# Kernel optimization log

Measured on AMD Instinct MI355X. Metric: run time of the kernel, lower is better.

The kernel has to match this reference:

```python
import jax, jax.numpy as jnp
import numpy as np

GAMMA = 0.99
GAE_LAMBDA = 0.95
SEQ_LEN = 1024
BATCH = 32768


def setup_inputs() -> dict:
    key = jax.random.key(0)
    k1, k2 = jax.random.split(key)
    rewards = jax.random.normal(k1, (SEQ_LEN, BATCH), dtype=jnp.float32)
    values = jax.random.normal(k2, (SEQ_LEN, BATCH), dtype=jnp.float32)
    return {"rewards": rewards, "values": values}


def _compute_advantages(rewards, values, gamma, gae_lambda):
    # delta_t = r_t + gamma * V_{t+1} - V_t  for t = 0 .. T-2  -> [T-1, B]
    deltas = rewards[:-1] + gamma * values[1:] - values[:-1]
    gl = gamma * gae_lambda

    def step(carry, delta):
        adv = delta + gl * carry
        return adv, adv

    init = jnp.zeros_like(deltas[0])
    # reverse scan implements the backward-in-time GAE recurrence
    _, advantages = jax.lax.scan(step, init, deltas, reverse=True)
    return advantages  # [T-1, B], equals torch advantages[:-1]


def reference(rewards, values):
    return _compute_advantages(rewards, values, GAMMA, GAE_LAMBDA)
```

## Files before the change

### kernel.cpp

```cpp
#include <hip/hip_runtime.h>


#define GAE_T 1024
#define GAE_B 32768

__global__ __launch_bounds__(64) void gae_scan_kernel(
    const float* __restrict__ rewards,
    const float* __restrict__ values,
    float* __restrict__ out) {
    const int b = blockIdx.x * blockDim.x + threadIdx.x;

    const float gamma = 0.99f;
    const float gl = (float)(0.99 * 0.95);

    const float* rp = rewards + b;
    const float* vp = values + b;
    float* op = out + b;

    float v_next = vp[(GAE_T - 1) * GAE_B];
    float adv = 0.0f;

    int t = GAE_T - 2;

    for (int k = 0; k < 7; ++k, --t) {
        float v = vp[t * GAE_B];
        float r = rp[t * GAE_B];
        adv = r + gamma * v_next - v + gl * adv;
        op[t * GAE_B] = adv;
        v_next = v;
    }

    for (; t >= 7; t -= 8) {
        float r8[8], v8[8];
#pragma unroll
        for (int k = 0; k < 8; ++k) {
            v8[k] = vp[(t - k) * GAE_B];
            r8[k] = rp[(t - k) * GAE_B];
        }
#pragma unroll
        for (int k = 0; k < 8; ++k) {
            float v = v8[k];
            adv = r8[k] + gamma * v_next - v + gl * adv;
            op[(t - k) * GAE_B] = adv;
            v_next = v;
        }
    }
}

extern "C" void kernel_launch(void* const* d_in, const int* in_sizes, int n_in,
                              void* d_out, int out_size, void* d_ws, size_t ws_size,
                              hipStream_t stream) {
    const float* rewards = (const float*)d_in[0];
    const float* values = (const float*)d_in[1];
    float* out = (float*)d_out;

    dim3 grid(GAE_B / 64);
    dim3 block(64);
    gae_scan_kernel<<<grid, block, 0, stream>>>(rewards, values, out);
}
```

Measured before the change: 363.8 us.

## Split time axis into chunks with three-pass scan for GAE

Replaces the per-column sequential scan with a chunked decomposition. Each chunk computes a local reverse scan and its aggregate, a combine kernel propagates carries across chunks, and a fixup kernel adds the decayed carry into each chunk's outputs. This exposes far more parallelism than one thread per column over 1023 serial steps, and float4 accesses widen the memory transactions. The cost is an extra read and write of the whole output plus workspace use, with a fallback to the single-pass kernel when workspace is too small.

```diff
diff --git a/kernel.cpp b/kernel.cpp
--- a/kernel.cpp
+++ b/kernel.cpp
@@ -1,60 +1,152 @@
 #include <hip/hip_runtime.h>
 
 
-#define GAE_T 1024
-#define GAE_B 32768
+#define GAE_T   1024
+#define GAE_B   32768
+#define GAE_T1  1023
+#define B4      (GAE_B / 4)
 
-__global__ __launch_bounds__(64) void gae_scan_kernel(
-    const float* __restrict__ rewards,
-    const float* __restrict__ values,
+#define GAMMA_F 0.99f
+#define GL_F    0.9405f
+
+#define GAE_STEP(r, v)                                      \
+  p.x = (r).x + GAMMA_F * vn.x - (v).x + GL_F * p.x;        \
+  p.y = (r).y + GAMMA_F * vn.y - (v).y + GL_F * p.y;        \
+  p.z = (r).z + GAMMA_F * vn.z - (v).z + GL_F * p.z;        \
+  p.w = (r).w + GAMMA_F * vn.w - (v).w + GL_F * p.w;
+
+__global__ __launch_bounds__(256) void gae_partial(
+    const float4* __restrict__ r4, const float4* __restrict__ v4,
+    float4* __restrict__ o4, float4* __restrict__ agg4, int S) {
+  const int q = blockIdx.x * 256 + threadIdx.x;
+  const int c = blockIdx.y;
+  const int t_lo = c * S;
+  int t_hi = t_lo + S - 1;
+  if (t_hi > GAE_T1 - 1) t_hi = GAE_T1 - 1;
+
+  float4 vn = v4[(t_hi + 1) * B4 + q];
+  float4 p = make_float4(0.f, 0.f, 0.f, 0.f);
+
+  int t = t_hi;
+  const int pre = (t_hi - t_lo + 1) & 3;
+  for (int k = 0; k < pre; ++k, --t) {
+    float4 r = r4[t * B4 + q];
+    float4 v = v4[t * B4 + q];
+    GAE_STEP(r, v)
+    o4[t * B4 + q] = p;
+    vn = v;
+  }
+  for (; t >= t_lo + 3; t -= 4) {
+    float4 r0 = r4[(t    ) * B4 + q], v0 = v4[(t    ) * B4 + q];
+    float4 r1 = r4[(t - 1) * B4 + q], v1 = v4[(t - 1) * B4 + q];
+    float4 r2 = r4[(t - 2) * B4 + q], v2 = v4[(t - 2) * B4 + q];
+    float4 r3 = r4[(t - 3) * B4 + q], v3 = v4[(t - 3) * B4 + q];
+    GAE_STEP(r0, v0)  o4[(t    ) * B4 + q] = p;  vn = v0;
+    GAE_STEP(r1, v1)  o4[(t - 1) * B4 + q] = p;  vn = v1;
+    GAE_STEP(r2, v2)  o4[(t - 2) * B4 + q] = p;  vn = v2;
+    GAE_STEP(r3, v3)  o4[(t - 3) * B4 + q] = p;  vn = v3;
+  }
+  agg4[c * B4 + q] = p;
+}
+
+__global__ __launch_bounds__(256) void gae_combine(
+    float* __restrict__ agg, int C, float gS) {
+  const int b = blockIdx.x * 256 + threadIdx.x;
+  float carry = 0.f;
+#pragma unroll 8
+  for (int c = C - 1; c >= 0; --c) {
+    float a = agg[c * GAE_B + b];
+    agg[c * GAE_B + b] = carry;
+    carry = a + gS * carry;
+  }
+}
+
+__global__ __launch_bounds__(256) void gae_fixup(
+    float4* __restrict__ o4, const float4* __restrict__ carry4, int S) {
+  const int q = blockIdx.x * 256 + threadIdx.x;
+  const int c = blockIdx.y;
+  const int t_lo = c * S;
+  const int t_hi = t_lo + S - 1;
+
+  float4 ci = carry4[c * B4 + q];
+  float4 x = make_float4(GL_F * ci.x, GL_F * ci.y, GL_F * ci.z, GL_F * ci.w);
+  for (int t = t_hi; t >= t_lo + 3; t -= 4) {
+    float4 o0 = o4[(t    ) * B4 + q];
+    float4 o1 = o4[(t - 1) * B4 + q];
+    float4 o2 = o4[(t - 2) * B4 + q];
+    float4 o3 = o4[(t - 3) * B4 + q];
+    o0.x += x.x; o0.y += x.y; o0.z += x.z; o0.w += x.w;
+    x.x *= GL_F; x.y *= GL_F; x.z *= GL_F; x.w *= GL_F;
+    o1.x += x.x; o1.y += x.y; o1.z += x.z; o1.w += x.w;
+    x.x *= GL_F; x.y *= GL_F; x.z *= GL_F; x.w *= GL_F;
+    o2.x += x.x; o2.y += x.y; o2.z += x.z; o2.w += x.w;
+    x.x *= GL_F; x.y *= GL_F; x.z *= GL_F; x.w *= GL_F;
+    o3.x += x.x; o3.y += x.y; o3.z += x.z; o3.w += x.w;
+    x.x *= GL_F; x.y *= GL_F; x.z *= GL_F; x.w *= GL_F;
+    o4[(t    ) * B4 + q] = o0;
+    o4[(t - 1) * B4 + q] = o1;
+    o4[(t - 2) * B4 + q] = o2;
+    o4[(t - 3) * B4 + q] = o3;
+  }
+}
+
+__global__ __launch_bounds__(64) void gae_single_pass(
+    const float* __restrict__ rewards, const float* __restrict__ values,
     float* __restrict__ out) {
-    const int b = blockIdx.x * blockDim.x + threadIdx.x;
-
-    const float gamma = 0.99f;
-    const float gl = (float)(0.99 * 0.95);
-
-    const float* rp = rewards + b;
-    const float* vp = values + b;
-    float* op = out + b;
-
-    float v_next = vp[(GAE_T - 1) * GAE_B];
-    float adv = 0.0f;
-
-    int t = GAE_T - 2;
-
-    for (int k = 0; k < 7; ++k, --t) {
-        float v = vp[t * GAE_B];
-        float r = rp[t * GAE_B];
-        adv = r + gamma * v_next - v + gl * adv;
-        op[t * GAE_B] = adv;
-        v_next = v;
+  const int b = blockIdx.x * blockDim.x + threadIdx.x;
+  const float* rp = rewards + b;
+  const float* vp = values + b;
+  float* op = out + b;
+  float vn = vp[(GAE_T - 1) * GAE_B];
+  float adv = 0.0f;
+  int t = GAE_T - 2;
+  for (int k = 0; k < 7; ++k, --t) {
+    float v = vp[t * GAE_B], r = rp[t * GAE_B];
+    adv = r + GAMMA_F * vn - v + GL_F * adv;
+    op[t * GAE_B] = adv;
+    vn = v;
+  }
+  for (; t >= 7; t -= 8) {
+    float r8[8], v8[8];
+#pragma unroll
+    for (int k = 0; k < 8; ++k) {
+      v8[k] = vp[(t - k) * GAE_B];
+      r8[k] = rp[(t - k) * GAE_B];
     }
-
-    for (; t >= 7; t -= 8) {
-        float r8[8], v8[8];
 #pragma unroll
-        for (int k = 0; k < 8; ++k) {
-            v8[k] = vp[(t - k) * GAE_B];
-            r8[k] = rp[(t - k) * GAE_B];
-        }
-#pragma unroll
-        for (int k = 0; k < 8; ++k) {
-            float v = v8[k];
-            adv = r8[k] + gamma * v_next - v + gl * adv;
-            op[(t - k) * GAE_B] = adv;
-            v_next = v;
-        }
+    for (int k = 0; k < 8; ++k) {
+      adv = r8[k] + GAMMA_F * vn - v8[k] + GL_F * adv;
+      op[(t - k) * GAE_B] = adv;
+      vn = v8[k];
     }
+  }
 }
 
 extern "C" void kernel_launch(void* const* d_in, const int* in_sizes, int n_in,
                               void* d_out, int out_size, void* d_ws, size_t ws_size,
                               hipStream_t stream) {
-    const float* rewards = (const float*)d_in[0];
-    const float* values = (const float*)d_in[1];
-    float* out = (float*)d_out;
+  const float* rewards = (const float*)d_in[0];
+  const float* values = (const float*)d_in[1];
+  float* out = (float*)d_out;
 
-    dim3 grid(GAE_B / 64);
-    dim3 block(64);
-    gae_scan_kernel<<<grid, block, 0, stream>>>(rewards, values, out);
+  int C = 32;
+  if (ws_size < (size_t)32 * GAE_B * 4) C = 16;
+  if (ws_size < (size_t)16 * GAE_B * 4) C = 8;
+  if (ws_size < (size_t)8 * GAE_B * 4) {
+    gae_single_pass<<<dim3(GAE_B / 64), dim3(64), 0, stream>>>(rewards, values, out);
+    return;
+  }
+  const int S = (GAE_T1 + C - 1) / C;
+
+  float gS = 1.f;
+  for (int i = 0; i < S; ++i) gS *= GL_F;
+
+  const float4* r4 = (const float4*)rewards;
+  const float4* v4 = (const float4*)values;
+  float4* o4 = (float4*)out;
+  float4* agg4 = (float4*)d_ws;
+
+  gae_partial<<<dim3(B4 / 256, C), dim3(256), 0, stream>>>(r4, v4, o4, agg4, S);
+  gae_combine<<<dim3(GAE_B / 256), dim3(256), 0, stream>>>((float*)d_ws, C, gS);
+  gae_fixup<<<dim3(B4 / 256, C - 1), dim3(256), 0, stream>>>(o4, agg4, S);
 }
```

Result: slower. 371.2 us (+2.0%).

## Split time axis across warps with chunked scan and carry fixup pass

Applied to the files above, without the earlier changes.

Replaces the one-thread-per-column serial backward scan with a chunked parallel scan. Each of 8 waves per block scans a 128-step time chunk, the chunk aggregates are combined through shared memory, and a second pass adds the decayed carry to outputs already written. Loads are vectorised to float2 and software-prefetched. This trades a long serial dependency chain and low parallelism for an extra read and write of the output. The fixup multiplies the carry by 1/gl at every step, which may cost some precision.

```diff
diff --git a/kernel.cpp b/kernel.cpp
--- a/kernel.cpp
+++ b/kernel.cpp
@@ -1,60 +1,123 @@
 #include <hip/hip_runtime.h>
+#include <math.h>
 
 
-#define GAE_T 1024
-#define GAE_B 32768
+#define T_OUT 1023
+#define B2    16384
+#define NW    8
+#define S_CH  128
 
-__global__ __launch_bounds__(64) void gae_scan_kernel(
-    const float* __restrict__ rewards,
-    const float* __restrict__ values,
-    float* __restrict__ out) {
-    const int b = blockIdx.x * blockDim.x + threadIdx.x;
+#define GAMMA_F 0.99f
+#define GL_F    0.9405f
+#define INVG_F  1.0632642212653909f
 
-    const float gamma = 0.99f;
-    const float gl = (float)(0.99 * 0.95);
+#define STEP2(r, v)                                \
+  p.x = (r).x + GAMMA_F * vn.x - (v).x + GL_F * p.x; \
+  p.y = (r).y + GAMMA_F * vn.y - (v).y + GL_F * p.y;
 
-    const float* rp = rewards + b;
-    const float* vp = values + b;
-    float* op = out + b;
+__global__ __launch_bounds__(512, 2) void gae_fused(
+    const float2* __restrict__ r2, const float2* __restrict__ v2,
+    float2* __restrict__ o2, float gS_full, float gS_last) {
+  __shared__ float2 aggs[NW][64];
 
-    float v_next = vp[(GAE_T - 1) * GAE_B];
-    float adv = 0.0f;
+  const int lane = threadIdx.x & 63;
+  const int w    = threadIdx.x >> 6;
+  const int q    = blockIdx.x * 64 + lane;
 
-    int t = GAE_T - 2;
+  const int t_lo = w * S_CH;
+  const int t_hi = (w == NW - 1) ? (T_OUT - 1) : (t_lo + S_CH - 1);
 
-    for (int k = 0; k < 7; ++k, --t) {
-        float v = vp[t * GAE_B];
-        float r = rp[t * GAE_B];
-        adv = r + gamma * v_next - v + gl * adv;
-        op[t * GAE_B] = adv;
-        v_next = v;
+  const float2* rp = r2 + q;
+  const float2* vp = v2 + q;
+  float2*       op = o2 + q;
+
+  float2 vn = vp[(t_hi + 1) * B2];
+  float2 p  = make_float2(0.f, 0.f);
+
+  int t = t_hi;
+  const int pre = (t_hi - t_lo + 1) & 3;
+  for (int k = 0; k < pre; ++k, --t) {
+    float2 r = rp[t * B2];
+    float2 v = vp[t * B2];
+    STEP2(r, v)
+    op[t * B2] = p;
+    vn = v;
+  }
+
+  {
+    float2 rc[4], vc[4];
+#pragma unroll
+    for (int k = 0; k < 4; ++k) { rc[k] = rp[(t - k) * B2]; vc[k] = vp[(t - k) * B2]; }
+    for (; t - 4 >= t_lo + 3; t -= 4) {
+      float2 rn_[4], vn_[4];
+#pragma unroll
+      for (int k = 0; k < 4; ++k) { rn_[k] = rp[(t - 4 - k) * B2]; vn_[k] = vp[(t - 4 - k) * B2]; }
+#pragma unroll
+      for (int k = 0; k < 4; ++k) {
+        STEP2(rc[k], vc[k])
+        op[(t - k) * B2] = p;
+        vn = vc[k];
+      }
+#pragma unroll
+      for (int k = 0; k < 4; ++k) { rc[k] = rn_[k]; vc[k] = vn_[k]; }
     }
+#pragma unroll
+    for (int k = 0; k < 4; ++k) {
+      STEP2(rc[k], vc[k])
+      op[(t - k) * B2] = p;
+      vn = vc[k];
+    }
+  }
 
-    for (; t >= 7; t -= 8) {
-        float r8[8], v8[8];
+  aggs[w][lane] = p;
+  __syncthreads();
+
+  float2 K = make_float2(0.f, 0.f);
+  for (int j = NW - 1; j > w; --j) {
+    const float gj = (j == NW - 1) ? gS_last : gS_full;
+    float2 a = aggs[j][lane];
+    K.x = a.x + gj * K.x;
+    K.y = a.y + gj * K.y;
+  }
+
+  if (w < NW - 1) {
+    float2 x = make_float2(gS_full * K.x, gS_full * K.y);
+    int u = t_lo;
+    float2 oc[4];
 #pragma unroll
-        for (int k = 0; k < 8; ++k) {
-            v8[k] = vp[(t - k) * GAE_B];
-            r8[k] = rp[(t - k) * GAE_B];
-        }
+    for (int k = 0; k < 4; ++k) oc[k] = op[(u + k) * B2];
+    for (; u + 4 <= t_hi - 3; u += 4) {
+      float2 on_[4];
 #pragma unroll
-        for (int k = 0; k < 8; ++k) {
-            float v = v8[k];
-            adv = r8[k] + gamma * v_next - v + gl * adv;
-            op[(t - k) * GAE_B] = adv;
-            v_next = v;
-        }
+      for (int k = 0; k < 4; ++k) on_[k] = op[(u + 4 + k) * B2];
+#pragma unroll
+      for (int k = 0; k < 4; ++k) {
+        oc[k].x += x.x; oc[k].y += x.y;
+        op[(u + k) * B2] = oc[k];
+        x.x *= INVG_F;  x.y *= INVG_F;
+      }
+#pragma unroll
+      for (int k = 0; k < 4; ++k) oc[k] = on_[k];
     }
+#pragma unroll
+    for (int k = 0; k < 4; ++k) {
+      oc[k].x += x.x; oc[k].y += x.y;
+      op[(u + k) * B2] = oc[k];
+      x.x *= INVG_F;  x.y *= INVG_F;
+    }
+  }
 }
 
 extern "C" void kernel_launch(void* const* d_in, const int* in_sizes, int n_in,
                               void* d_out, int out_size, void* d_ws, size_t ws_size,
                               hipStream_t stream) {
-    const float* rewards = (const float*)d_in[0];
-    const float* values = (const float*)d_in[1];
-    float* out = (float*)d_out;
+  const float2* r2 = (const float2*)d_in[0];
+  const float2* v2 = (const float2*)d_in[1];
+  float2* o2 = (float2*)d_out;
 
-    dim3 grid(GAE_B / 64);
-    dim3 block(64);
-    gae_scan_kernel<<<grid, block, 0, stream>>>(rewards, values, out);
+  const double g = (double)GL_F;
+  const float gS_full = (float)pow(g, 128);
+  const float gS_last = (float)pow(g, 127);
+
+  gae_fused<<<dim3(B2 / 64), dim3(512), 0, stream>>>(r2, v2, o2, gS_full, gS_last);
 }
```

After: 361.3 us. About the same (-0.7%).
